# Performance work log

Measured on AMD Instinct MI355X. Metric: run time of the kernel, lower is better.

The kernel has to match this reference:

```python
import jax, jax.numpy as jnp
import numpy as np

N_NODES = 524288
NUM_GRAPHS = 8192
H = 256


def setup_inputs() -> dict:
    key = jax.random.key(0)
    ks = jax.random.split(key, 16)
    def lin(k, fan_in, fan_out):
        kw, kb = jax.random.split(k)
        bound = 1.0 / np.sqrt(fan_in)
        W = jax.random.uniform(kw, (fan_in, fan_out), jnp.float32, -bound, bound)
        b = jax.random.uniform(kb, (fan_out,), jnp.float32, -bound, bound)
        return W, b
    x = jax.random.normal(ks[0], (N_NODES, H), jnp.float32)
    batch = jnp.sort(jax.random.randint(ks[1], (N_NODES,), 0, NUM_GRAPHS, jnp.int64))
    W_att1, b_att1 = lin(ks[2], H, H // 2)
    W_att2, b_att2 = lin(ks[3], H // 2, 1)
    Wm, bm = lin(ks[4], H, H)
    Wx, bx = lin(ks[5], H, H)
    Ww, bw = lin(ks[6], H, H)
    Wc1, bc1 = lin(ks[7], 3 * H, 2 * H)
    Wc2, bc2 = lin(ks[8], 2 * H, H)
    gamma = jnp.ones((H,), jnp.float32)
    beta = jnp.zeros((H,), jnp.float32)
    return dict(x=x, batch=batch, W_att1=W_att1, b_att1=b_att1, W_att2=W_att2,
                b_att2=b_att2, Wm=Wm, bm=bm, Wx=Wx, bx=bx, Ww=Ww, bw=bw,
                Wc1=Wc1, bc1=bc1, Wc2=Wc2, bc2=bc2, gamma=gamma, beta=beta)


def reference(x, batch, W_att1, b_att1, W_att2, b_att2, Wm, bm, Wx, bx, Ww, bw,
              Wc1, bc1, Wc2, bc2, gamma, beta):
    # --- node attention scores: Linear -> tanh -> Linear -> squeeze ---
    s = (jnp.tanh(x @ W_att1 + b_att1) @ W_att2 + b_att2)[:, 0]  # [N]
    # --- segment softmax over graphs (numerically stable) ---
    smax = jax.ops.segment_max(s, batch, num_segments=NUM_GRAPHS)    # [G]
    e = jnp.exp(s - smax[batch])
    denom = jax.ops.segment_sum(e, batch, num_segments=NUM_GRAPHS)   # [G]
    w = e / denom[batch]                                             # [N]
    # --- scatter pools ---
    h_weighted = jax.ops.segment_sum(w[:, None] * x, batch, num_segments=NUM_GRAPHS)  # [G,H]
    sums = jax.ops.segment_sum(x, batch, num_segments=NUM_GRAPHS)
    counts = jax.ops.segment_sum(jnp.ones((x.shape[0],), x.dtype), batch, num_segments=NUM_GRAPHS)
    h_mean = sums / jnp.maximum(counts, 1.0)[:, None]
    h_max = jax.ops.segment_max(x, batch, num_segments=NUM_GRAPHS)
    h_max = jnp.where(counts[:, None] > 0, h_max, 0.0)
    # --- dense tail ---
    h_mean = h_mean @ Wm + bm
    h_max = h_max @ Wx + bx
    h_weighted = h_weighted @ Ww + bw
    combined = jnp.concatenate([h_mean, h_max, h_weighted], axis=-1)  # [G,3H]
    out = jax.nn.gelu(combined @ Wc1 + bc1, approximate=False) @ Wc2 + bc2
    # LayerNorm (eps matches torch default 1e-5); dropout inactive (eval)
    mu = out.mean(-1, keepdims=True)
    var = out.var(-1, keepdims=True)
    out = (out - mu) / jnp.sqrt(var + 1e-5) * gamma + beta
    return out
```

## Files before the change

### kernel.cpp

```cpp
#include <hip/hip_runtime.h>
#include <hip/hip_bf16.h>

#define N_NODES 524288
#define NUM_G   8192
#define HDIM    256

#define NCACHE  112
#define SMAXROW 256

typedef short v8s __attribute__((ext_vector_type(8)));
typedef float v4f __attribute__((ext_vector_type(4)));
using bf16 = __hip_bfloat16;

static __device__ __forceinline__ unsigned short f2b(float f) {
    unsigned u = __builtin_bit_cast(unsigned, f);
    u += 0x7FFFu + ((u >> 16) & 1u);
    return (unsigned short)(u >> 16);
}
static __device__ __forceinline__ float b2f(unsigned short s) {
    unsigned u = ((unsigned)s) << 16;
    return __builtin_bit_cast(float, u);
}

__global__ __launch_bounds__(256) void swizzle_kernel(const float* __restrict__ W,
                                                      unsigned short* __restrict__ out,
                                                      int K, int N) {
    int idx = blockIdx.x * 256 + threadIdx.x;
    int NT = N >> 4;
    int total = (K >> 5) * NT * 64;
    if (idx >= total) return;
    int lane = idx & 63;
    int t = idx >> 6;
    int nt = t % NT;
    int ks = t / NT;
    int colIdx = nt * 16 + (lane & 15);
    int k0 = ks * 32 + ((lane >> 4) << 3);
    v8s v;
#pragma unroll
    for (int j = 0; j < 8; ++j) v[j] = (short)f2b(W[(long long)(k0 + j) * N + colIdx]);
    *(v8s*)(out + (long long)idx * 8) = v;
}

__global__ __launch_bounds__(256) void offsets_kernel(const int* __restrict__ batch,
                                                      int* __restrict__ offs) {
    int g = blockIdx.x * 256 + threadIdx.x;
    if (g > NUM_G) return;
    int stride = (batch[N_NODES - 1] == 0) ? 2 : 1;
    if (g == NUM_G) { offs[NUM_G] = N_NODES; return; }
    int lo = 0, hi = N_NODES;
    while (lo < hi) {
        int mid = (lo + hi) >> 1;
        if (batch[(long long)mid * stride] < g) lo = mid + 1; else hi = mid;
    }
    offs[g] = lo;
}

static __device__ __forceinline__ float block_sum(float v) {
    __shared__ float sm[4];
#pragma unroll
    for (int off = 32; off > 0; off >>= 1) v += __shfl_xor(v, off);
    if ((threadIdx.x & 63) == 0) sm[threadIdx.x >> 6] = v;
    __syncthreads();
    v = sm[0] + sm[1] + sm[2] + sm[3];
    __syncthreads();
    return v;
}
static __device__ __forceinline__ float block_max(float v) {
    __shared__ float sm[4];
#pragma unroll
    for (int off = 32; off > 0; off >>= 1) v = fmaxf(v, __shfl_xor(v, off));
    if ((threadIdx.x & 63) == 0) sm[threadIdx.x >> 6] = v;
    __syncthreads();
    v = fmaxf(fmaxf(sm[0], sm[1]), fmaxf(sm[2], sm[3]));
    __syncthreads();
    return v;
}

__global__ __launch_bounds__(256) void fused_pool_kernel(const float* __restrict__ x,
                                                         const unsigned short* __restrict__ W1sw,
                                                         const float* __restrict__ b1,
                                                         const float* __restrict__ w2,
                                                         const float* __restrict__ b2,
                                                         const int* __restrict__ offs,
                                                         unsigned short* __restrict__ pooled) {
    __shared__ unsigned short xls[NCACHE * 256];
    __shared__ float spart[4][SMAXROW];
    __shared__ float wrow[SMAXROW];

    int g = blockIdx.x;
    int tid = threadIdx.x;
    int wv = tid >> 6, lane = tid & 63;
    int col = lane & 15, quad = lane >> 4;
    int beg = offs[g], end = offs[g + 1];
    int n = end - beg;
    long long prow = (long long)g * 768;
    if (n <= 0) {
        pooled[prow + tid] = 0;
        pooled[prow + 256 + tid] = 0;
        pooled[prow + 512 + tid] = 0;
        return;
    }
    int neff = n > SMAXROW ? SMAXROW : n;
    int ncache = neff > NCACHE ? NCACHE : neff;
    int ntile = (neff + 15) >> 4;

    {
        int rb = tid >> 5;
        int sc = tid & 31;
        const float* xg = x + (long long)beg * 256 + sc * 8;
        for (int base = 0; base < ncache; base += 32) {
            float4 f[8];
#pragma unroll
            for (int rr = 0; rr < 4; ++rr) {
                int r = base + rr * 8 + rb;
                if (r < ncache) {
                    const float4* p = (const float4*)(xg + (long long)r * 256);
                    f[rr * 2] = p[0];
                    f[rr * 2 + 1] = p[1];
                }
            }
#pragma unroll
            for (int rr = 0; rr < 4; ++rr) {
                int r = base + rr * 8 + rb;
                if (r < ncache) {
                    v8s v;
                    v[0] = (short)f2b(f[rr * 2].x); v[1] = (short)f2b(f[rr * 2].y);
                    v[2] = (short)f2b(f[rr * 2].z); v[3] = (short)f2b(f[rr * 2].w);
                    v[4] = (short)f2b(f[rr * 2 + 1].x); v[5] = (short)f2b(f[rr * 2 + 1].y);
                    v[6] = (short)f2b(f[rr * 2 + 1].z); v[7] = (short)f2b(f[rr * 2 + 1].w);
                    *(v8s*)(xls + r * 256 + ((sc ^ (r & 31)) << 3)) = v;
                }
            }
        }
    }
    __syncthreads();

    v8s bfr0[8], bfr1[8];
#pragma unroll
    for (int ks = 0; ks < 8; ++ks) {
        bfr0[ks] = *(const v8s*)(W1sw + ((long long)(ks * 8 + wv * 2 + 0) * 64 + lane) * 8);
        bfr1[ks] = *(const v8s*)(W1sw + ((long long)(ks * 8 + wv * 2 + 1) * 64 + lane) * 8);
    }
    float b1v0 = b1[(wv * 2 + 0) * 16 + col], w2v0 = w2[(wv * 2 + 0) * 16 + col];
    float b1v1 = b1[(wv * 2 + 1) * 16 + col], w2v1 = w2[(wv * 2 + 1) * 16 + col];
    float b2v = b2[0];

    for (int tile = 0; tile < ntile; ++tile) {
        int row = tile * 16 + col;
        v8s a[8];
        if ((tile + 1) * 16 <= ncache) {
#pragma unroll
            for (int ks = 0; ks < 8; ++ks)
                a[ks] = *(const v8s*)(xls + row * 256 + ((((ks << 2) + quad) ^ (row & 31)) << 3));
        } else {
#pragma unroll
            for (int ks = 0; ks < 8; ++ks) {
                v8s av = {};
                if (row < ncache) {
                    av = *(const v8s*)(xls + row * 256 + ((((ks << 2) + quad) ^ (row & 31)) << 3));
                } else if (row < neff) {
                    const float4* p = (const float4*)(x + (long long)(beg + row) * 256 + ks * 32 + quad * 8);
                    float4 f0 = p[0], f1 = p[1];
                    av[0] = (short)f2b(f0.x); av[1] = (short)f2b(f0.y);
                    av[2] = (short)f2b(f0.z); av[3] = (short)f2b(f0.w);
                    av[4] = (short)f2b(f1.x); av[5] = (short)f2b(f1.y);
                    av[6] = (short)f2b(f1.z); av[7] = (short)f2b(f1.w);
                }
                a[ks] = av;
            }
        }
        v4f acc0 = {}, acc1 = {};
#pragma unroll
        for (int ks = 0; ks < 8; ++ks) {
            acc0 = __builtin_amdgcn_mfma_f32_16x16x32_bf16(a[ks], bfr0[ks], acc0, 0, 0, 0);
            acc1 = __builtin_amdgcn_mfma_f32_16x16x32_bf16(a[ks], bfr1[ks], acc1, 0, 0, 0);
        }
        float p[4];
#pragma unroll
        for (int r = 0; r < 4; ++r)
            p[r] = tanhf(acc0[r] + b1v0) * w2v0 + tanhf(acc1[r] + b1v1) * w2v1;
#pragma unroll
        for (int off = 1; off < 16; off <<= 1) {
#pragma unroll
            for (int r = 0; r < 4; ++r) p[r] += __shfl_xor(p[r], off);
        }
        if (col == 0) {
            int rb2 = tile * 16 + quad * 4;
#pragma unroll
            for (int r = 0; r < 4; ++r) spart[wv][rb2 + r] = p[r];
        }
    }
    __syncthreads();

    float myS = spart[0][tid] + spart[1][tid] + spart[2][tid] + spart[3][tid] + b2v;
    bool valid = (tid < neff);
    float m = block_max(valid ? myS : -3.0e38f);
    float e = valid ? __expf(myS - m) : 0.f;
    float d = block_sum(e);
    wrow[tid] = e / d;
    __syncthreads();

    float asum = 0.f, awsum = 0.f, amax = -3.0e38f;
    int sbase = tid >> 3, within = tid & 7;
    for (int r = 0; r < ncache; ++r) {
        float wg = wrow[r];
        float xv = b2f(xls[r * 256 + ((sbase ^ (r & 31)) << 3) + within]);
        asum += xv;
        awsum += wg * xv;
        amax = fmaxf(amax, xv);
    }
    for (int r = ncache; r < n; ++r) {
        float wg = (r < SMAXROW) ? wrow[r] : 0.f;
        float xv = x[(long long)(beg + r) * 256 + tid];
        asum += xv;
        awsum += wg * xv;
        amax = fmaxf(amax, xv);
    }
    pooled[prow + tid]       = f2b(asum / (float)n);
    pooled[prow + 256 + tid] = f2b(amax);
    pooled[prow + 512 + tid] = f2b(awsum);
}

__global__ __launch_bounds__(256) void wfuse_gemm(const float* __restrict__ Wm,
                                                  const float* __restrict__ Wx,
                                                  const float* __restrict__ Ww,
                                                  const unsigned short* __restrict__ Wc1sw,
                                                  float* __restrict__ Wbig) {
    int tid = threadIdx.x;
    int wv = tid >> 6, lane = tid & 63;
    int col = lane & 15, quad = lane >> 4;
    int mbase = blockIdx.x * 64 + wv * 16;
    int nbase = blockIdx.y * 64;
    int p = mbase >> 8;
    const float* A = (p == 0) ? Wm : ((p == 1) ? Wx : Ww);
    int arow = (mbase & 255) + col;
    const unsigned short* Bs = Wc1sw + (size_t)p * 8 * 32 * 64 * 8;

    v4f acc[4] = {};
    for (int ks = 0; ks < 8; ++ks) {
        const float4* ap = (const float4*)(A + (long long)arow * 256 + ks * 32 + quad * 8);
        float4 f0 = ap[0], f1 = ap[1];
        v8s a;
        a[0] = (short)f2b(f0.x); a[1] = (short)f2b(f0.y);
        a[2] = (short)f2b(f0.z); a[3] = (short)f2b(f0.w);
        a[4] = (short)f2b(f1.x); a[5] = (short)f2b(f1.y);
        a[6] = (short)f2b(f1.z); a[7] = (short)f2b(f1.w);
#pragma unroll
        for (int nt = 0; nt < 4; ++nt) {
            int ntg = (nbase >> 4) + nt;
            v8s b = *(const v8s*)(Bs + ((long long)(ks * 32 + ntg) * 64 + lane) * 8);
            acc[nt] = __builtin_amdgcn_mfma_f32_16x16x32_bf16(a, b, acc[nt], 0, 0, 0);
        }
    }
#pragma unroll
    for (int nt = 0; nt < 4; ++nt) {
#pragma unroll
        for (int r = 0; r < 4; ++r)
            Wbig[(long long)(mbase + quad * 4 + r) * 512 + nbase + nt * 16 + col] = acc[nt][r];
    }
}

__global__ __launch_bounds__(256) void bfuse_kernel(const float* __restrict__ bm,
                                                    const float* __restrict__ bx,
                                                    const float* __restrict__ bw,
                                                    const float* __restrict__ Wc1,
                                                    const float* __restrict__ bc1,
                                                    float* __restrict__ bfused) {
    __shared__ float sm2[4][64];
    int tid = threadIdx.x;
    int j = blockIdx.x * 64 + (tid & 63);
    int kq = tid >> 6;
    float acc = 0.f;
    for (int k = kq * 64; k < kq * 64 + 64; ++k) {
        acc += bm[k] * Wc1[(long long)k * 512 + j];
        acc += bx[k] * Wc1[(long long)(256 + k) * 512 + j];
        acc += bw[k] * Wc1[(long long)(512 + k) * 512 + j];
    }
    sm2[kq][tid & 63] = acc;
    __syncthreads();
    if (kq == 0) bfused[j] = sm2[0][tid] + sm2[1][tid] + sm2[2][tid] + sm2[3][tid] + bc1[j];
}

__global__ __launch_bounds__(256) void gemm_kernel(const unsigned short* __restrict__ A, int lda,
                                                   const unsigned short* __restrict__ Bsw,
                                                   const float* __restrict__ bias,
                                                   void* __restrict__ C, int ldc,
                                                   int K, int N, int mode) {
    int tid = threadIdx.x;
    int wave = tid >> 6, lane = tid & 63;
    int col = lane & 15, quad = lane >> 4;
    int mbase = blockIdx.x * 64 + wave * 16;
    int nbase = blockIdx.y * 64;
    int NT = N >> 4;
    int nks = K >> 5;

    v4f acc[4] = {};
    for (int ks = 0; ks < nks; ++ks) {
        v8s a = *(const v8s*)(A + (long long)(mbase + col) * lda + ks * 32 + quad * 8);
#pragma unroll
        for (int nt = 0; nt < 4; ++nt) {
            int ntg = (nbase >> 4) + nt;
            v8s b = *(const v8s*)(Bsw + ((long long)(ks * NT + ntg) * 64 + lane) * 8);
            acc[nt] = __builtin_amdgcn_mfma_f32_16x16x32_bf16(a, b, acc[nt], 0, 0, 0);
        }
    }
#pragma unroll
    for (int nt = 0; nt < 4; ++nt) {
#pragma unroll
        for (int r = 0; r < 4; ++r) {
            int row = mbase + quad * 4 + r;
            int cidx = nbase + nt * 16 + col;
            float v = acc[nt][r] + bias[cidx];
            if (mode == 1) v = 0.5f * v * (1.0f + erff(v * 0.70710678118654752f));
            if (mode == 2) ((float*)C)[(long long)row * ldc + cidx] = v;
            else ((unsigned short*)C)[(long long)row * ldc + cidx] = f2b(v);
        }
    }
}

__global__ __launch_bounds__(256) void ln_kernel(const float* __restrict__ pre,
                                                 const float* __restrict__ gamma,
                                                 const float* __restrict__ beta,
                                                 float* __restrict__ out) {
    int g = blockIdx.x, t = threadIdx.x;
    float v = pre[(long long)g * 256 + t];
    float mu = block_sum(v) * (1.0f / 256.0f);
    float dv = v - mu;
    float var = block_sum(dv * dv) * (1.0f / 256.0f);
    float rstd = rsqrtf(var + 1e-5f);
    out[(long long)g * 256 + t] = dv * rstd * gamma[t] + beta[t];
}

extern "C" void kernel_launch(void* const* d_in, const int* in_sizes, int n_in,
                              void* d_out, int out_size, void* d_ws, size_t ws_size,
                              hipStream_t stream) {
    const float* x      = (const float*)d_in[0];
    const int*   batch  = (const int*)d_in[1];
    const float* W_att1 = (const float*)d_in[2];
    const float* b_att1 = (const float*)d_in[3];
    const float* W_att2 = (const float*)d_in[4];
    const float* b_att2 = (const float*)d_in[5];
    const float* Wm     = (const float*)d_in[6];
    const float* bm     = (const float*)d_in[7];
    const float* Wx     = (const float*)d_in[8];
    const float* bx     = (const float*)d_in[9];
    const float* Ww     = (const float*)d_in[10];
    const float* bw     = (const float*)d_in[11];
    const float* Wc1    = (const float*)d_in[12];
    const float* bc1    = (const float*)d_in[13];
    const float* Wc2    = (const float*)d_in[14];
    const float* bc2    = (const float*)d_in[15];
    const float* gamma  = (const float*)d_in[16];
    const float* beta   = (const float*)d_in[17];
    float* out = (float*)d_out;

    char* ws = (char*)d_ws;
    size_t cur = 0;
    auto alloc = [&](size_t bytes) -> char* {
        char* p = ws + cur;
        cur += (bytes + 255) & ~(size_t)255;
        return p;
    };
    int*            offs     = (int*)  alloc((size_t)(NUM_G + 1) * 4);
    unsigned short* pooled   = (unsigned short*)alloc((size_t)NUM_G * 768 * 2);
    unsigned short* hidden   = (unsigned short*)alloc((size_t)NUM_G * 512 * 2);
    float*          pre      = (float*)alloc((size_t)NUM_G * 256 * 4);
    unsigned short* W1sw     = (unsigned short*)alloc((size_t)8  * 8  * 64 * 8 * 2);
    unsigned short* Wc1sw    = (unsigned short*)alloc((size_t)24 * 32 * 64 * 8 * 2);
    unsigned short* Wc2sw    = (unsigned short*)alloc((size_t)16 * 16 * 64 * 8 * 2);
    float*          Wbig     = (float*)alloc((size_t)768 * 512 * 4);
    unsigned short* Wbigsw   = (unsigned short*)alloc((size_t)24 * 32 * 64 * 8 * 2);
    float*          bfused   = (float*)alloc((size_t)512 * 4);

    auto swz = [&](const float* W, unsigned short* o, int K, int N) {
        int total = (K >> 5) * (N >> 4) * 64;
        swizzle_kernel<<<(total + 255) / 256, 256, 0, stream>>>(W, o, K, N);
    };

    swz(W_att1, W1sw, 256, 128);
    offsets_kernel<<<(NUM_G + 1 + 255) / 256, 256, 0, stream>>>(batch, offs);
    fused_pool_kernel<<<NUM_G, 256, 0, stream>>>(x, W1sw, b_att1, W_att2, b_att2, offs, pooled);

    swz(Wc1, Wc1sw, 768, 512);
    dim3 gw(12, 8);
    wfuse_gemm<<<gw, 256, 0, stream>>>(Wm, Wx, Ww, Wc1sw, Wbig);
    swz(Wbig, Wbigsw, 768, 512);
    bfuse_kernel<<<8, 256, 0, stream>>>(bm, bx, bw, Wc1, bc1, bfused);
    swz(Wc2, Wc2sw, 512, 256);

    dim3 g1(NUM_G / 64, 512 / 64);
    gemm_kernel<<<g1, 256, 0, stream>>>(pooled, 768, Wbigsw, bfused, (void*)hidden, 512, 768, 512, 1);
    dim3 g2(NUM_G / 64, 256 / 64);
    gemm_kernel<<<g2, 256, 0, stream>>>(hidden, 512, Wc2sw, bc2, (void*)pre, 256, 512, 256, 2);

    ln_kernel<<<NUM_G, 256, 0, stream>>>(pre, gamma, beta, out);
}
```

Baseline: 874.6 us.

## Merge prep kernels, restructure pooling with fused softmax, fuse GEMM2 with LayerNorm

```diff
diff --git a/kernel.cpp b/kernel.cpp
--- a/kernel.cpp
+++ b/kernel.cpp
@@ -5,12 +5,11 @@
 #define NUM_G   8192
 #define HDIM    256
 
-#define NCACHE  112
+#define NCACHE  72
 #define SMAXROW 256
 
 typedef short v8s __attribute__((ext_vector_type(8)));
 typedef float v4f __attribute__((ext_vector_type(4)));
-using bf16 = __hip_bfloat16;
 
 static __device__ __forceinline__ unsigned short f2b(float f) {
     unsigned u = __builtin_bit_cast(unsigned, f);
@@ -22,270 +21,274 @@
     return __builtin_bit_cast(float, u);
 }
 
-__global__ __launch_bounds__(256) void swizzle_kernel(const float* __restrict__ W,
-                                                      unsigned short* __restrict__ out,
-                                                      int K, int N) {
-    int idx = blockIdx.x * 256 + threadIdx.x;
-    int NT = N >> 4;
-    int total = (K >> 5) * NT * 64;
-    if (idx >= total) return;
-    int lane = idx & 63;
-    int t = idx >> 6;
-    int nt = t % NT;
-    int ks = t / NT;
-    int colIdx = nt * 16 + (lane & 15);
-    int k0 = ks * 32 + ((lane >> 4) << 3);
-    v8s v;
-#pragma unroll
-    for (int j = 0; j < 8; ++j) v[j] = (short)f2b(W[(long long)(k0 + j) * N + colIdx]);
-    *(v8s*)(out + (long long)idx * 8) = v;
-}
-
-__global__ __launch_bounds__(256) void offsets_kernel(const int* __restrict__ batch,
-                                                      int* __restrict__ offs) {
-    int g = blockIdx.x * 256 + threadIdx.x;
-    if (g > NUM_G) return;
-    int stride = (batch[N_NODES - 1] == 0) ? 2 : 1;
-    if (g == NUM_G) { offs[NUM_G] = N_NODES; return; }
-    int lo = 0, hi = N_NODES;
-    while (lo < hi) {
-        int mid = (lo + hi) >> 1;
-        if (batch[(long long)mid * stride] < g) lo = mid + 1; else hi = mid;
-    }
-    offs[g] = lo;
-}
-
-static __device__ __forceinline__ float block_sum(float v) {
-    __shared__ float sm[4];
-#pragma unroll
-    for (int off = 32; off > 0; off >>= 1) v += __shfl_xor(v, off);
-    if ((threadIdx.x & 63) == 0) sm[threadIdx.x >> 6] = v;
-    __syncthreads();
-    v = sm[0] + sm[1] + sm[2] + sm[3];
-    __syncthreads();
-    return v;
-}
-static __device__ __forceinline__ float block_max(float v) {
-    __shared__ float sm[4];
-#pragma unroll
-    for (int off = 32; off > 0; off >>= 1) v = fmaxf(v, __shfl_xor(v, off));
-    if ((threadIdx.x & 63) == 0) sm[threadIdx.x >> 6] = v;
-    __syncthreads();
-    v = fmaxf(fmaxf(sm[0], sm[1]), fmaxf(sm[2], sm[3]));
-    __syncthreads();
-    return v;
-}
-
-__global__ __launch_bounds__(256) void fused_pool_kernel(const float* __restrict__ x,
-                                                         const unsigned short* __restrict__ W1sw,
-                                                         const float* __restrict__ b1,
-                                                         const float* __restrict__ w2,
-                                                         const float* __restrict__ b2,
-                                                         const int* __restrict__ offs,
-                                                         unsigned short* __restrict__ pooled) {
+__global__ __launch_bounds__(256) void prep_kernel(
+    const float* __restrict__ W_att1, unsigned short* __restrict__ W1sw,
+    const float* __restrict__ Wc2,    unsigned short* __restrict__ Wc2sw,
+    const int*   __restrict__ batch,  int* __restrict__ offs,
+    const float* __restrict__ Wm, const float* __restrict__ Wx, const float* __restrict__ Ww,
+    const float* __restrict__ Wc1, unsigned short* __restrict__ Wbigsw,
+    const float* __restrict__ bm, const float* __restrict__ bx, const float* __restrict__ bw,
+    const float* __restrict__ bc1, float* __restrict__ bfused)
+{
+    __shared__ float tileS[64][65];
+    __shared__ float sm2[4][64];
+    int b = blockIdx.x, tid = threadIdx.x;
+
+    if (b < 80) {
+        const float* W; unsigned short* o; int K, N, blk;
+        if (b < 16) { W = W_att1; o = W1sw; K = 256; N = 128; blk = b; }
+        else        { W = Wc2;    o = Wc2sw; K = 512; N = 256; blk = b - 16; }
+        int idx = blk * 256 + tid;
+        int NT = N >> 4;
+        int total = (K >> 5) * NT * 64;
+        if (idx < total) {
+            int lane = idx & 63;
+            int t = idx >> 6;
+            int nt = t % NT, ks = t / NT;
+            int colIdx = nt * 16 + (lane & 15);
+            int k0 = ks * 32 + ((lane >> 4) << 3);
+            v8s v;
+#pragma unroll
+            for (int j = 0; j < 8; ++j) v[j] = (short)f2b(W[(long long)(k0 + j) * N + colIdx]);
+            *(v8s*)(o + (long long)idx * 8) = v;
+        }
+    } else if (b < 113) {
+        int g = (b - 80) * 256 + tid;
+        if (g <= NUM_G) {
+            int stride = (batch[N_NODES - 1] == 0) ? 2 : 1;
+            if (g == NUM_G) { offs[NUM_G] = N_NODES; }
+            else {
+                int lo = 0, hi = N_NODES;
+                while (lo < hi) {
+                    int mid = (lo + hi) >> 1;
+                    if (batch[(long long)mid * stride] < g) lo = mid + 1; else hi = mid;
+                }
+                offs[g] = lo;
+            }
+        }
+    } else if (b < 209) {
+        int local = b - 113;
+        int bx_ = local % 12, by_ = local / 12;
+        int wv = tid >> 6, lane = tid & 63;
+        int col = lane & 15, quad = lane >> 4;
+        int mbase = bx_ * 64 + wv * 16;
+        int nbase = by_ * 64;
+        int p = mbase >> 8;
+        const float* A = (p == 0) ? Wm : ((p == 1) ? Wx : Ww);
+        int arow = (mbase & 255) + col;
+
+        v4f acc[4] = {};
+        for (int ks = 0; ks < 8; ++ks) {
+            const float4* ap = (const float4*)(A + (long long)arow * 256 + ks * 32 + quad * 8);
+            float4 f0 = ap[0], f1 = ap[1];
+            v8s a;
+            a[0] = (short)f2b(f0.x); a[1] = (short)f2b(f0.y);
+            a[2] = (short)f2b(f0.z); a[3] = (short)f2b(f0.w);
+            a[4] = (short)f2b(f1.x); a[5] = (short)f2b(f1.y);
+            a[6] = (short)f2b(f1.z); a[7] = (short)f2b(f1.w);
+            int krow = p * 256 + ks * 32 + ((lane >> 4) << 3);
+#pragma unroll
+            for (int nt = 0; nt < 4; ++nt) {
+                int bcol = nbase + nt * 16 + (lane & 15);
+                v8s bb;
+#pragma unroll
+                for (int j = 0; j < 8; ++j) bb[j] = (short)f2b(Wc1[(long long)(krow + j) * 512 + bcol]);
+                acc[nt] = __builtin_amdgcn_mfma_f32_16x16x32_bf16(a, bb, acc[nt], 0, 0, 0);
+            }
+        }
+#pragma unroll
+        for (int nt = 0; nt < 4; ++nt)
+#pragma unroll
+            for (int r = 0; r < 4; ++r)
+                tileS[wv * 16 + quad * 4 + r][nt * 16 + col] = acc[nt][r];
+        __syncthreads();
+        for (int o = tid; o < 512; o += 256) {
+            int ksl = o >> 8, rem = o & 255;
+            int ntl = rem >> 6, ln = rem & 63;
+            int colw = ntl * 16 + (ln & 15);
+            int row0 = ksl * 32 + ((ln >> 4) << 3);
+            int mb0 = (b - 113) % 12 * 64;
+            v8s v;
+#pragma unroll
+            for (int j = 0; j < 8; ++j) v[j] = (short)f2b(tileS[row0 + j][colw]);
+            int ks_g = (mb0 >> 5) + ksl;
+            int nt_g = (nbase >> 4) + ntl;
+            *(v8s*)(Wbigsw + ((long long)(ks_g * 32 + nt_g) * 64 + ln) * 8) = v;
+        }
+    } else {
+        int j = (b - 209) * 64 + (tid & 63);
+        int kq = tid >> 6;
+        float acc = 0.f;
+        for (int k = kq * 64; k < kq * 64 + 64; ++k) {
+            acc += bm[k] * Wc1[(long long)k * 512 + j];
+            acc += bx[k] * Wc1[(long long)(256 + k) * 512 + j];
+            acc += bw[k] * Wc1[(long long)(512 + k) * 512 + j];
+        }
+        sm2[kq][tid & 63] = acc;
+        __syncthreads();
+        if (kq == 0) bfused[j] = sm2[0][tid] + sm2[1][tid] + sm2[2][tid] + sm2[3][tid] + bc1[j];
+    }
+}
+
+__global__ __launch_bounds__(256, 4) void fused_pool_kernel(
+    const float* __restrict__ x,
+    const unsigned short* __restrict__ W1sw,
+    const float* __restrict__ b1,
+    const float* __restrict__ w2,
+    const float* __restrict__ b2,
+    const int* __restrict__ offs,
+    unsigned short* __restrict__ pooled)
+{
     __shared__ unsigned short xls[NCACHE * 256];
-    __shared__ float spart[4][SMAXROW];
-    __shared__ float wrow[SMAXROW];
-
-    int g = blockIdx.x;
-    int tid = threadIdx.x;
+    __shared__ float els[SMAXROW];
+    __shared__ float wden[4];
+
+    int g = blockIdx.x, tid = threadIdx.x;
     int wv = tid >> 6, lane = tid & 63;
     int col = lane & 15, quad = lane >> 4;
     int beg = offs[g], end = offs[g + 1];
     int n = end - beg;
     long long prow = (long long)g * 768;
     if (n <= 0) {
-        pooled[prow + tid] = 0;
-        pooled[prow + 256 + tid] = 0;
-        pooled[prow + 512 + tid] = 0;
+        pooled[prow + tid] = 0; pooled[prow + 256 + tid] = 0; pooled[prow + 512 + tid] = 0;
         return;
     }
     int neff = n > SMAXROW ? SMAXROW : n;
     int ncache = neff > NCACHE ? NCACHE : neff;
     int ntile = (neff + 15) >> 4;
-
+    float b2v = b2[0];
+    int sc = lane & 31, half = lane >> 5;
+
+    float dsum = 0.f;
+    for (int t = wv; t < ntile; t += 4) {
+        int r0 = t * 16;
+        int rend = (r0 + 16 < ncache) ? r0 + 16 : ncache;
+#pragma unroll
+        for (int rr = 0; rr < 8; ++rr) {
+            int row = r0 + rr * 2 + half;
+            if (row < rend) {
+                const float4* p = (const float4*)(x + (long long)(beg + row) * HDIM + sc * 8);
+                float4 f0 = p[0], f1 = p[1];
+                v8s v;
+                v[0] = (short)f2b(f0.x); v[1] = (short)f2b(f0.y);
+                v[2] = (short)f2b(f0.z); v[3] = (short)f2b(f0.w);
+                v[4] = (short)f2b(f1.x); v[5] = (short)f2b(f1.y);
+                v[6] = (short)f2b(f1.z); v[7] = (short)f2b(f1.w);
+                *(v8s*)(xls + row * 256 + ((sc ^ (row & 31)) << 3)) = v;
+            }
+        }
+        int rowf = r0 + col;
+        v8s a[8];
+        if (rowf < ncache) {
+#pragma unroll
+            for (int ks = 0; ks < 8; ++ks)
+                a[ks] = *(const v8s*)(xls + rowf * 256 + ((((ks << 2) + quad) ^ (rowf & 31)) << 3));
+        } else if (rowf < neff) {
+#pragma unroll
+            for (int ks = 0; ks < 8; ++ks) {
+                const float4* p = (const float4*)(x + (long long)(beg + rowf) * HDIM + ks * 32 + quad * 8);
+                float4 f0 = p[0], f1 = p[1];
+                v8s av;
+                av[0] = (short)f2b(f0.x); av[1] = (short)f2b(f0.y);
+                av[2] = (short)f2b(f0.z); av[3] = (short)f2b(f0.w);
+                av[4] = (short)f2b(f1.x); av[5] = (short)f2b(f1.y);
+                av[6] = (short)f2b(f1.z); av[7] = (short)f2b(f1.w);
+                a[ks] = av;
+            }
+        } else {
+#pragma unroll
+            for (int ks = 0; ks < 8; ++ks) a[ks] = (v8s){0, 0, 0, 0, 0, 0, 0, 0};
+        }
+        v4f acc[8] = {};
+#pragma unroll
+        for (int ks = 0; ks < 8; ++ks)
+#pragma unroll
+            for (int jt = 0; jt < 8; ++jt) {
+                v8s bb = *(const v8s*)(W1sw + ((long long)(ks * 8 + jt) * 64 + lane) * 8);
+                acc[jt] = __builtin_amdgcn_mfma_f32_16x16x32_bf16(a[ks], bb, acc[jt], 0, 0, 0);
+            }
+        float pr[4];
+#pragma unroll
+        for (int r = 0; r < 4; ++r) {
+            float s = 0.f;
+#pragma unroll
+            for (int jt = 0; jt < 8; ++jt) {
+                int j = jt * 16 + col;
+                s += tanhf(acc[jt][r] + b1[j]) * w2[j];
+            }
+            pr[r] = s;
+        }
+#pragma unroll
+        for (int off = 1; off < 16; off <<= 1)
+#pragma unroll
+            for (int r = 0; r < 4; ++r) pr[r] += __shfl_xor(pr[r], off);
+        if (col == 0) {
+#pragma unroll
+            for (int r = 0; r < 4; ++r) {
+                int re = r0 + quad * 4 + r;
+                if (re < neff) {
+                    float e = __expf(pr[r] + b2v);
+                    els[re] = e;
+                    dsum += e;
+                }
+            }
+        }
+    }
+#pragma unroll
+    for (int off = 1; off < 64; off <<= 1) dsum += __shfl_xor(dsum, off);
+    if (lane == 0) wden[wv] = dsum;
+    __syncthreads();
+    float invd = 1.0f / (wden[0] + wden[1] + wden[2] + wden[3]);
+
+    float as[4] = {0, 0, 0, 0}, aw[4] = {0, 0, 0, 0};
+    float am[4] = {-3.0e38f, -3.0e38f, -3.0e38f, -3.0e38f};
+    for (int r = wv; r < n; r += 4) {
+        if (r < ncache) {
+            float e = els[r];
+            int rx = r & 31;
+#pragma unroll
+            for (int q = 0; q < 4; ++q) {
+                int c = lane + 64 * q;
+                float xv = b2f(xls[r * 256 + (((c >> 3) ^ rx) << 3) + (c & 7)]);
+                as[q] += xv; aw[q] += e * xv; am[q] = fmaxf(am[q], xv);
+            }
+        } else {
+            float e = (r < neff) ? els[r] : 0.f;
+            const float* xr = x + (long long)(beg + r) * HDIM;
+#pragma unroll
+            for (int q = 0; q < 4; ++q) {
+                float xv = xr[lane + 64 * q];
+                as[q] += xv; aw[q] += e * xv; am[q] = fmaxf(am[q], xv);
+            }
+        }
+    }
+    __syncthreads();
+    float* comb = (float*)xls;
+#pragma unroll
+    for (int q = 0; q < 4; ++q) {
+        int c = lane + 64 * q;
+        comb[0 * 1024 + wv * 256 + c] = as[q];
+        comb[1 * 1024 + wv * 256 + c] = aw[q];
+        comb[2 * 1024 + wv * 256 + c] = am[q];
+    }
+    __syncthreads();
     {
-        int rb = tid >> 5;
-        int sc = tid & 31;
-        const float* xg = x + (long long)beg * 256 + sc * 8;
-        for (int base = 0; base < ncache; base += 32) {
-            float4 f[8];
-#pragma unroll
-            for (int rr = 0; rr < 4; ++rr) {
-                int r = base + rr * 8 + rb;
-                if (r < ncache) {
-                    const float4* p = (const float4*)(xg + (long long)r * 256);
-                    f[rr * 2] = p[0];
-                    f[rr * 2 + 1] = p[1];
-                }
-            }
-#pragma unroll
-            for (int rr = 0; rr < 4; ++rr) {
-                int r = base + rr * 8 + rb;
-                if (r < ncache) {
-                    v8s v;
-                    v[0] = (short)f2b(f[rr * 2].x); v[1] = (short)f2b(f[rr * 2].y);
-                    v[2] = (short)f2b(f[rr * 2].z); v[3] = (short)f2b(f[rr * 2].w);
-                    v[4] = (short)f2b(f[rr * 2 + 1].x); v[5] = (short)f2b(f[rr * 2 + 1].y);
-                    v[6] = (short)f2b(f[rr * 2 + 1].z); v[7] = (short)f2b(f[rr * 2 + 1].w);
-                    *(v8s*)(xls + r * 256 + ((sc ^ (r & 31)) << 3)) = v;
-                }
-            }
-        }
-    }
-    __syncthreads();
-
-    v8s bfr0[8], bfr1[8];
-#pragma unroll
-    for (int ks = 0; ks < 8; ++ks) {
-        bfr0[ks] = *(const v8s*)(W1sw + ((long long)(ks * 8 + wv * 2 + 0) * 64 + lane) * 8);
-        bfr1[ks] = *(const v8s*)(W1sw + ((long long)(ks * 8 + wv * 2 + 1) * 64 + lane) * 8);
-    }
-    float b1v0 = b1[(wv * 2 + 0) * 16 + col], w2v0 = w2[(wv * 2 + 0) * 16 + col];
-    float b1v1 = b1[(wv * 2 + 1) * 16 + col], w2v1 = w2[(wv * 2 + 1) * 16 + col];
-    float b2v = b2[0];
-
-    for (int tile = 0; tile < ntile; ++tile) {
-        int row = tile * 16 + col;
-        v8s a[8];
-        if ((tile + 1) * 16 <= ncache) {
-#pragma unroll
-            for (int ks = 0; ks < 8; ++ks)
-                a[ks] = *(const v8s*)(xls + row * 256 + ((((ks << 2) + quad) ^ (row & 31)) << 3));
-        } else {
-#pragma unroll
-            for (int ks = 0; ks < 8; ++ks) {
-                v8s av = {};
-                if (row < ncache) {
-                    av = *(const v8s*)(xls + row * 256 + ((((ks << 2) + quad) ^ (row & 31)) << 3));
-                } else if (row < neff) {
-                    const float4* p = (const float4*)(x + (long long)(beg + row) * 256 + ks * 32 + quad * 8);
-                    float4 f0 = p[0], f1 = p[1];
-                    av[0] = (short)f2b(f0.x); av[1] = (short)f2b(f0.y);
-                    av[2] = (short)f2b(f0.z); av[3] = (short)f2b(f0.w);
-                    av[4] = (short)f2b(f1.x); av[5] = (short)f2b(f1.y);
-                    av[6] = (short)f2b(f1.z); av[7] = (short)f2b(f1.w);
-                }
-                a[ks] = av;
-            }
-        }
-        v4f acc0 = {}, acc1 = {};
-#pragma unroll
-        for (int ks = 0; ks < 8; ++ks) {
-            acc0 = __builtin_amdgcn_mfma_f32_16x16x32_bf16(a[ks], bfr0[ks], acc0, 0, 0, 0);
-            acc1 = __builtin_amdgcn_mfma_f32_16x16x32_bf16(a[ks], bfr1[ks], acc1, 0, 0, 0);
-        }
-        float p[4];
-#pragma unroll
-        for (int r = 0; r < 4; ++r)
-            p[r] = tanhf(acc0[r] + b1v0) * w2v0 + tanhf(acc1[r] + b1v1) * w2v1;
-#pragma unroll
-        for (int off = 1; off < 16; off <<= 1) {
-#pragma unroll
-            for (int r = 0; r < 4; ++r) p[r] += __shfl_xor(p[r], off);
-        }
-        if (col == 0) {
-            int rb2 = tile * 16 + quad * 4;
-#pragma unroll
-            for (int r = 0; r < 4; ++r) spart[wv][rb2 + r] = p[r];
-        }
-    }
-    __syncthreads();
-
-    float myS = spart[0][tid] + spart[1][tid] + spart[2][tid] + spart[3][tid] + b2v;
-    bool valid = (tid < neff);
-    float m = block_max(valid ? myS : -3.0e38f);
-    float e = valid ? __expf(myS - m) : 0.f;
-    float d = block_sum(e);
-    wrow[tid] = e / d;
-    __syncthreads();
-
-    float asum = 0.f, awsum = 0.f, amax = -3.0e38f;
-    int sbase = tid >> 3, within = tid & 7;
-    for (int r = 0; r < ncache; ++r) {
-        float wg = wrow[r];
-        float xv = b2f(xls[r * 256 + ((sbase ^ (r & 31)) << 3) + within]);
-        asum += xv;
-        awsum += wg * xv;
-        amax = fmaxf(amax, xv);
-    }
-    for (int r = ncache; r < n; ++r) {
-        float wg = (r < SMAXROW) ? wrow[r] : 0.f;
-        float xv = x[(long long)(beg + r) * 256 + tid];
-        asum += xv;
-        awsum += wg * xv;
-        amax = fmaxf(amax, xv);
-    }
-    pooled[prow + tid]       = f2b(asum / (float)n);
-    pooled[prow + 256 + tid] = f2b(amax);
-    pooled[prow + 512 + tid] = f2b(awsum);
-}
-
-__global__ __launch_bounds__(256) void wfuse_gemm(const float* __restrict__ Wm,
-                                                  const float* __restrict__ Wx,
-                                                  const float* __restrict__ Ww,
-                                                  const unsigned short* __restrict__ Wc1sw,
-                                                  float* __restrict__ Wbig) {
-    int tid = threadIdx.x;
-    int wv = tid >> 6, lane = tid & 63;
-    int col = lane & 15, quad = lane >> 4;
-    int mbase = blockIdx.x * 64 + wv * 16;
-    int nbase = blockIdx.y * 64;
-    int p = mbase >> 8;
-    const float* A = (p == 0) ? Wm : ((p == 1) ? Wx : Ww);
-    int arow = (mbase & 255) + col;
-    const unsigned short* Bs = Wc1sw + (size_t)p * 8 * 32 * 64 * 8;
-
-    v4f acc[4] = {};
-    for (int ks = 0; ks < 8; ++ks) {
-        const float4* ap = (const float4*)(A + (long long)arow * 256 + ks * 32 + quad * 8);
-        float4 f0 = ap[0], f1 = ap[1];
-        v8s a;
-        a[0] = (short)f2b(f0.x); a[1] = (short)f2b(f0.y);
-        a[2] = (short)f2b(f0.z); a[3] = (short)f2b(f0.w);
-        a[4] = (short)f2b(f1.x); a[5] = (short)f2b(f1.y);
-        a[6] = (short)f2b(f1.z); a[7] = (short)f2b(f1.w);
-#pragma unroll
-        for (int nt = 0; nt < 4; ++nt) {
-            int ntg = (nbase >> 4) + nt;
-            v8s b = *(const v8s*)(Bs + ((long long)(ks * 32 + ntg) * 64 + lane) * 8);
-            acc[nt] = __builtin_amdgcn_mfma_f32_16x16x32_bf16(a, b, acc[nt], 0, 0, 0);
-        }
-    }
-#pragma unroll
-    for (int nt = 0; nt < 4; ++nt) {
-#pragma unroll
-        for (int r = 0; r < 4; ++r)
-            Wbig[(long long)(mbase + quad * 4 + r) * 512 + nbase + nt * 16 + col] = acc[nt][r];
-    }
-}
-
-__global__ __launch_bounds__(256) void bfuse_kernel(const float* __restrict__ bm,
-                                                    const float* __restrict__ bx,
-                                                    const float* __restrict__ bw,
-                                                    const float* __restrict__ Wc1,
-                                                    const float* __restrict__ bc1,
-                                                    float* __restrict__ bfused) {
-    __shared__ float sm2[4][64];
-    int tid = threadIdx.x;
-    int j = blockIdx.x * 64 + (tid & 63);
-    int kq = tid >> 6;
-    float acc = 0.f;
-    for (int k = kq * 64; k < kq * 64 + 64; ++k) {
-        acc += bm[k] * Wc1[(long long)k * 512 + j];
-        acc += bx[k] * Wc1[(long long)(256 + k) * 512 + j];
-        acc += bw[k] * Wc1[(long long)(512 + k) * 512 + j];
-    }
-    sm2[kq][tid & 63] = acc;
-    __syncthreads();
-    if (kq == 0) bfused[j] = sm2[0][tid] + sm2[1][tid] + sm2[2][tid] + sm2[3][tid] + bc1[j];
+        int c = tid;
+        float s0 = comb[c] + comb[256 + c] + comb[512 + c] + comb[768 + c];
+        float s1 = comb[1024 + c] + comb[1280 + c] + comb[1536 + c] + comb[1792 + c];
+        float m0 = fmaxf(fmaxf(comb[2048 + c], comb[2304 + c]),
+                         fmaxf(comb[2560 + c], comb[2816 + c]));
+        pooled[prow + c]       = f2b(s0 / (float)n);
+        pooled[prow + 256 + c] = f2b(m0);
+        pooled[prow + 512 + c] = f2b(s1 * invd);
+    }
 }
 
 __global__ __launch_bounds__(256) void gemm_kernel(const unsigned short* __restrict__ A, int lda,
                                                    const unsigned short* __restrict__ Bsw,
                                                    const float* __restrict__ bias,
-                                                   void* __restrict__ C, int ldc,
-                                                   int K, int N, int mode) {
+                                                   unsigned short* __restrict__ C, int ldc,
+                                                   int K, int N) {
     int tid = threadIdx.x;
     int wave = tid >> 6, lane = tid & 63;
     int col = lane & 15, quad = lane >> 4;
@@ -305,30 +308,71 @@
         }
     }
 #pragma unroll
-    for (int nt = 0; nt < 4; ++nt) {
+    for (int nt = 0; nt < 4; ++nt)
 #pragma unroll
         for (int r = 0; r < 4; ++r) {
             int row = mbase + quad * 4 + r;
             int cidx = nbase + nt * 16 + col;
             float v = acc[nt][r] + bias[cidx];
-            if (mode == 1) v = 0.5f * v * (1.0f + erff(v * 0.70710678118654752f));
-            if (mode == 2) ((float*)C)[(long long)row * ldc + cidx] = v;
-            else ((unsigned short*)C)[(long long)row * ldc + cidx] = f2b(v);
-        }
-    }
-}
-
-__global__ __launch_bounds__(256) void ln_kernel(const float* __restrict__ pre,
-                                                 const float* __restrict__ gamma,
-                                                 const float* __restrict__ beta,
-                                                 float* __restrict__ out) {
-    int g = blockIdx.x, t = threadIdx.x;
-    float v = pre[(long long)g * 256 + t];
-    float mu = block_sum(v) * (1.0f / 256.0f);
-    float dv = v - mu;
-    float var = block_sum(dv * dv) * (1.0f / 256.0f);
-    float rstd = rsqrtf(var + 1e-5f);
-    out[(long long)g * 256 + t] = dv * rstd * gamma[t] + beta[t];
+            v = 0.5f * v * (1.0f + erff(v * 0.70710678118654752f));
+            C[(long long)row * ldc + cidx] = f2b(v);
+        }
+}
+
+__global__ __launch_bounds__(256) void gemm2ln_kernel(const unsigned short* __restrict__ A,
+                                                      const unsigned short* __restrict__ Bsw,
+                                                      const float* __restrict__ bias,
+                                                      const float* __restrict__ gamma,
+                                                      const float* __restrict__ beta,
+                                                      float* __restrict__ out) {
+    int tid = threadIdx.x;
+    int wv = tid >> 6, lane = tid & 63;
+    int col = lane & 15, quad = lane >> 4;
+    int mbase = blockIdx.x * 64 + wv * 16;
+
+    v4f acc[16] = {};
+    for (int ks = 0; ks < 16; ++ks) {
+        v8s a = *(const v8s*)(A + (long long)(mbase + col) * 512 + ks * 32 + quad * 8);
+#pragma unroll
+        for (int nt = 0; nt < 16; ++nt) {
+            v8s b = *(const v8s*)(Bsw + ((long long)(ks * 16 + nt) * 64 + lane) * 8);
+            acc[nt] = __builtin_amdgcn_mfma_f32_16x16x32_bf16(a, b, acc[nt], 0, 0, 0);
+        }
+    }
+    float vsum[4] = {0, 0, 0, 0};
+#pragma unroll
+    for (int nt = 0; nt < 16; ++nt) {
+        float bv = bias[nt * 16 + col];
+#pragma unroll
+        for (int r = 0; r < 4; ++r) { acc[nt][r] += bv; vsum[r] += acc[nt][r]; }
+    }
+#pragma unroll
+    for (int off = 1; off < 16; off <<= 1)
+#pragma unroll
+        for (int r = 0; r < 4; ++r) vsum[r] += __shfl_xor(vsum[r], off);
+    float mu[4], sq[4] = {0, 0, 0, 0};
+#pragma unroll
+    for (int r = 0; r < 4; ++r) mu[r] = vsum[r] * (1.0f / 256.0f);
+#pragma unroll
+    for (int nt = 0; nt < 16; ++nt)
+#pragma unroll
+        for (int r = 0; r < 4; ++r) { float d = acc[nt][r] - mu[r]; sq[r] += d * d; }
+#pragma unroll
+    for (int off = 1; off < 16; off <<= 1)
+#pragma unroll
+        for (int r = 0; r < 4; ++r) sq[r] += __shfl_xor(sq[r], off);
+    float rstd[4];
+#pragma unroll
+    for (int r = 0; r < 4; ++r) rstd[r] = rsqrtf(sq[r] * (1.0f / 256.0f) + 1e-5f);
+#pragma unroll
+    for (int nt = 0; nt < 16; ++nt) {
+        float gv = gamma[nt * 16 + col], bt = beta[nt * 16 + col];
+#pragma unroll
+        for (int r = 0; r < 4; ++r) {
+            int row = mbase + quad * 4 + r;
+            out[(long long)row * 256 + nt * 16 + col] = (acc[nt][r] - mu[r]) * rstd[r] * gv + bt;
+        }
+    }
 }
 
 extern "C" void kernel_launch(void* const* d_in, const int* in_sizes, int n_in,
@@ -361,37 +405,22 @@
         cur += (bytes + 255) & ~(size_t)255;
         return p;
     };
-    int*            offs     = (int*)  alloc((size_t)(NUM_G + 1) * 4);
-    unsigned short* pooled   = (unsigned short*)alloc((size_t)NUM_G * 768 * 2);
-    unsigned short* hidden   = (unsigned short*)alloc((size_t)NUM_G * 512 * 2);
-    float*          pre      = (float*)alloc((size_t)NUM_G * 256 * 4);
-    unsigned short* W1sw     = (unsigned short*)alloc((size_t)8  * 8  * 64 * 8 * 2);
-    unsigned short* Wc1sw    = (unsigned short*)alloc((size_t)24 * 32 * 64 * 8 * 2);
-    unsigned short* Wc2sw    = (unsigned short*)alloc((size_t)16 * 16 * 64 * 8 * 2);
-    float*          Wbig     = (float*)alloc((size_t)768 * 512 * 4);
-    unsigned short* Wbigsw   = (unsigned short*)alloc((size_t)24 * 32 * 64 * 8 * 2);
-    float*          bfused   = (float*)alloc((size_t)512 * 4);
-
-    auto swz = [&](const float* W, unsigned short* o, int K, int N) {
-        int total = (K >> 5) * (N >> 4) * 64;
-        swizzle_kernel<<<(total + 255) / 256, 256, 0, stream>>>(W, o, K, N);
-    };
-
-    swz(W_att1, W1sw, 256, 128);
-    offsets_kernel<<<(NUM_G + 1 + 255) / 256, 256, 0, stream>>>(batch, offs);
+    int*            offs   = (int*)alloc((size_t)(NUM_G + 1) * 4);
+    unsigned short* pooled = (unsigned short*)alloc((size_t)NUM_G * 768 * 2);
+    unsigned short* hidden = (unsigned short*)alloc((size_t)NUM_G * 512 * 2);
+    unsigned short* W1sw   = (unsigned short*)alloc((size_t)8  * 8  * 64 * 8 * 2);
+    unsigned short* Wc2sw  = (unsigned short*)alloc((size_t)16 * 16 * 64 * 8 * 2);
+    unsigned short* Wbigsw = (unsigned short*)alloc((size_t)24 * 32 * 64 * 8 * 2);
+    float*          bfused = (float*)alloc((size_t)512 * 4);
+
+    prep_kernel<<<217, 256, 0, stream>>>(W_att1, W1sw, Wc2, Wc2sw, batch, offs,
+                                         Wm, Wx, Ww, Wc1, Wbigsw,
+                                         bm, bx, bw, bc1, bfused);
+
     fused_pool_kernel<<<NUM_G, 256, 0, stream>>>(x, W1sw, b_att1, W_att2, b_att2, offs, pooled);
 
-    swz(Wc1, Wc1sw, 768, 512);
-    dim3 gw(12, 8);
-    wfuse_gemm<<<gw, 256, 0, stream>>>(Wm, Wx, Ww, Wc1sw, Wbig);
-    swz(Wbig, Wbigsw, 768, 512);
-    bfuse_kernel<<<8, 256, 0, stream>>>(bm, bx, bw, Wc1, bc1, bfused);
-    swz(Wc2, Wc2sw, 512, 256);
-
     dim3 g1(NUM_G / 64, 512 / 64);
-    gemm_kernel<<<g1, 256, 0, stream>>>(pooled, 768, Wbigsw, bfused, (void*)hidden, 512, 768, 512, 1);
-    dim3 g2(NUM_G / 64, 256 / 64);
-    gemm_kernel<<<g2, 256, 0, stream>>>(hidden, 512, Wc2sw, bc2, (void*)pre, 256, 512, 256, 2);
-
-    ln_kernel<<<NUM_G, 256, 0, stream>>>(pre, gamma, beta, out);
-}
+    gemm_kernel<<<g1, 256, 0, stream>>>(pooled, 768, Wbigsw, bfused, hidden, 512, 768, 512);
+
+    gemm2ln_kernel<<<NUM_G / 64, 256, 0, stream>>>(hidden, Wc2sw, bc2, gamma, beta, out);
+}
```

Measured after the change: 1.803 ms. 106% more time.
